# Performance work log

Measured on AMD Instinct MI355X. Metric: run time of the kernel, lower is better.

## Reference

```python
import jax, jax.numpy as jnp
import numpy as np

N_ETYPES = 6
N_STEPS = 5
N_ITERS = 6
N_LSTM_LAYERS = 3
NODES_PER_GRAPH = 200


def _uinit(key, shape, fan_in):
    s = 1.0 / np.sqrt(fan_in)
    return jax.random.uniform(key, shape, jnp.float32, -s, s)


def setup_inputs() -> dict:
    key = jax.random.key(0)
    ks = jax.random.split(key, 24)
    N, D = 64000, 64
    G = N // NODES_PER_GRAPH  # 320 graphs
    E = N * 16  # 1,024,000 edges
    feats = jax.random.normal(ks[0], (N, D), jnp.float32)
    # within-graph edges: local endpoint + graph offset
    graph_of_edge = jnp.repeat(jnp.arange(G, dtype=jnp.int32), E // G)
    src = jax.random.randint(ks[1], (E,), 0, NODES_PER_GRAPH, jnp.int32) + graph_of_edge * NODES_PER_GRAPH
    dst = jax.random.randint(ks[2], (E,), 0, NODES_PER_GRAPH, jnp.int32) + graph_of_edge * NODES_PER_GRAPH
    etypes = jax.random.randint(ks[3], (E,), 0, N_ETYPES, jnp.int32)
    node_graph = jnp.repeat(jnp.arange(G, dtype=jnp.int32), NODES_PER_GRAPH)
    # GatedGraphConv params: per-etype Linear(D,D) + GRUCell(D,D) (torch gate order r,z,n)
    W_edge = _uinit(ks[4], (N_ETYPES, D, D), D)
    b_edge = _uinit(ks[5], (N_ETYPES, D), D)
    gru_W_ih = _uinit(ks[6], (3 * D, D), D)
    gru_W_hh = _uinit(ks[7], (3 * D, D), D)
    gru_b_ih = _uinit(ks[8], (3 * D,), D)
    gru_b_hh = _uinit(ks[9], (3 * D,), D)
    # Set2Set LSTM: 3 layers, input 2D (layer0) / D (layers 1,2), hidden D; torch gate order i,f,g,o
    lstm_W_ih0 = _uinit(ks[10], (4 * D, 2 * D), D)
    lstm_W_hh0 = _uinit(ks[11], (4 * D, D), D)
    lstm_b_ih0 = _uinit(ks[12], (4 * D,), D)
    lstm_b_hh0 = _uinit(ks[13], (4 * D,), D)
    lstm_W_ih1 = _uinit(ks[14], (4 * D, D), D)
    lstm_W_hh1 = _uinit(ks[15], (4 * D, D), D)
    lstm_b_ih1 = _uinit(ks[16], (4 * D,), D)
    lstm_b_hh1 = _uinit(ks[17], (4 * D,), D)
    lstm_W_ih2 = _uinit(ks[18], (4 * D, D), D)
    lstm_W_hh2 = _uinit(ks[19], (4 * D, D), D)
    lstm_b_ih2 = _uinit(ks[20], (4 * D,), D)
    lstm_b_hh2 = _uinit(ks[21], (4 * D,), D)
    Wp = _uinit(ks[22], (3, 2 * D), 2 * D)
    bp = _uinit(ks[23], (3,), 2 * D)
    return dict(feats=feats, W_edge=W_edge, b_edge=b_edge,
                gru_W_ih=gru_W_ih, gru_W_hh=gru_W_hh, gru_b_ih=gru_b_ih, gru_b_hh=gru_b_hh,
                lstm_W_ih0=lstm_W_ih0, lstm_W_hh0=lstm_W_hh0, lstm_b_ih0=lstm_b_ih0, lstm_b_hh0=lstm_b_hh0,
                lstm_W_ih1=lstm_W_ih1, lstm_W_hh1=lstm_W_hh1, lstm_b_ih1=lstm_b_ih1, lstm_b_hh1=lstm_b_hh1,
                lstm_W_ih2=lstm_W_ih2, lstm_W_hh2=lstm_W_hh2, lstm_b_ih2=lstm_b_ih2, lstm_b_hh2=lstm_b_hh2,
                Wp=Wp, bp=bp, src=src, dst=dst, etypes=etypes, node_graph=node_graph)


def _ggnn_forward(feats, W_edge, b_edge, gru_W_ih, gru_W_hh, gru_b_ih, gru_b_hh,
                  lstm_params, Wp, bp, src, dst, etypes, node_graph):
    N, D = feats.shape
    G = N // NODES_PER_GRAPH
    h = feats
    # --- GatedGraphConv: 5 steps of etype-typed transform + scatter-sum + GRU ---
    for _ in range(N_STEPS):
        # transform every node by every etype weight (cheap: N << E), then gather per edge
        Wh = jnp.einsum('nd,tdo->tno', h, W_edge) + b_edge[:, None, :]  # [T,N,D]
        msg = Wh[etypes, src]                                           # [E,D] gather
        a = jax.ops.segment_sum(msg, dst, num_segments=N)               # [N,D] scatter-add
        gi = a @ gru_W_ih.T + gru_b_ih
        gh = h @ gru_W_hh.T + gru_b_hh
        i_r, i_z, i_n = jnp.split(gi, 3, -1)
        h_r, h_z, h_n = jnp.split(gh, 3, -1)
        r = jax.nn.sigmoid(i_r + h_r)
        z = jax.nn.sigmoid(i_z + h_z)
        n = jnp.tanh(i_n + r * h_n)
        h = (1.0 - z) * n + z * h
    feat = h
    # --- Set2Set readout ---
    q_star = jnp.zeros((G, 2 * D), feat.dtype)
    hs = jnp.zeros((N_LSTM_LAYERS, G, D), feat.dtype)
    cs = jnp.zeros((N_LSTM_LAYERS, G, D), feat.dtype)
    for _ in range(N_ITERS):
        x = q_star
        new_h, new_c = [], []
        for l, (Wi, Whh, bi, bh) in enumerate(lstm_params):
            gates = x @ Wi.T + bi + hs[l] @ Whh.T + bh
            ii, ff, gg, oo = jnp.split(gates, 4, -1)
            c = jax.nn.sigmoid(ff) * cs[l] + jax.nn.sigmoid(ii) * jnp.tanh(gg)
            x = jax.nn.sigmoid(oo) * jnp.tanh(c)
            new_h.append(x)
            new_c.append(c)
        hs = jnp.stack(new_h)
        cs = jnp.stack(new_c)
        q = x  # [G,D]
        e = jnp.sum(feat * q[node_graph], axis=-1)                         # [N]
        emax = jax.ops.segment_max(e, node_graph, num_segments=G)
        ex = jnp.exp(e - emax[node_graph])
        denom = jax.ops.segment_sum(ex, node_graph, num_segments=G)
        alpha = ex / denom[node_graph]                                     # segment softmax
        readout = jax.ops.segment_sum(feat * alpha[:, None], node_graph, num_segments=G)
        q_star = jnp.concatenate([q, readout], axis=-1)
    return q_star @ Wp.T + bp  # [G,3]


def reference(feats, W_edge, b_edge, gru_W_ih, gru_W_hh, gru_b_ih, gru_b_hh,
              lstm_W_ih0, lstm_W_hh0, lstm_b_ih0, lstm_b_hh0,
              lstm_W_ih1, lstm_W_hh1, lstm_b_ih1, lstm_b_hh1,
              lstm_W_ih2, lstm_W_hh2, lstm_b_ih2, lstm_b_hh2,
              Wp, bp, src, dst, etypes, node_graph):
    lstm_params = [
        (lstm_W_ih0, lstm_W_hh0, lstm_b_ih0, lstm_b_hh0),
        (lstm_W_ih1, lstm_W_hh1, lstm_b_ih1, lstm_b_hh1),
        (lstm_W_ih2, lstm_W_hh2, lstm_b_ih2, lstm_b_hh2),
    ]
    return _ggnn_forward(feats, W_edge, b_edge, gru_W_ih, gru_W_hh, gru_b_ih, gru_b_hh,
                         lstm_params, Wp, bp, src, dst, etypes, node_graph)
```

## Files before the change

### kernel.cpp

```cpp
#include <hip/hip_runtime.h>

typedef unsigned short u16;
typedef unsigned int u32;

#define DIM 64
#define NGRAPH 320
#define NPG 200
#define EPG 3200
#define EPG_P 5120
#define NSTEPS 5
#define NITERS 6
#define NTILES 13
#define NPAD 208
#define NTHR 1024

typedef __attribute__((ext_vector_type(8))) short bf16x8;
typedef __attribute__((ext_vector_type(4))) float f32x4;

__device__ __forceinline__ float bf2f(u16 u) {
  u32 x = ((u32)u) << 16;
  float f;
  __builtin_memcpy(&f, &x, 4);
  return f;
}
__device__ __forceinline__ u16 f2bf(float f) {
  u32 x;
  __builtin_memcpy(&x, &f, 4);
  x = (x + 0x7FFFu + ((x >> 16) & 1u)) >> 16;
  return (u16)x;
}
__device__ __forceinline__ float bflo(u32 w) {
  u32 x = w << 16;
  float f;
  __builtin_memcpy(&f, &x, 4);
  return f;
}
__device__ __forceinline__ float bfhi(u32 w) {
  u32 x = w & 0xffff0000u;
  float f;
  __builtin_memcpy(&f, &x, 4);
  return f;
}
__device__ __forceinline__ float sigmf(float x) { return 1.0f / (1.0f + __expf(-x)); }
__device__ __forceinline__ int swz(int row, int col) { return row * 64 + (col ^ ((row & 7) << 3)); }


__global__ void __launch_bounds__(256) k_csr(const int* __restrict__ src,
                                             const int* __restrict__ dst,
                                             const int* __restrict__ ety,
                                             u16* __restrict__ recs,
                                             int* __restrict__ rows) {
  __shared__ int cnt[3 * NPG];
  __shared__ int rofs[3 * (NPG + 1)];
  int g = blockIdx.x, tid = threadIdx.x;
  int base = g * NPG;
  for (int i = tid; i < 3 * NPG; i += 256) cnt[i] = 0;
  __syncthreads();
  for (int e = tid; e < EPG; e += 256) {
    int d = dst[g * EPG + e] - base;
    int t = ety[g * EPG + e];
    atomicAdd(&cnt[(t >> 1) * NPG + d], 1);
  }
  __syncthreads();
  if (tid == 0) {
    int s = 0;
    for (int p = 0; p < 3; p++) {
      for (int n = 0; n < NPG; n++) {
        rofs[p * (NPG + 1) + n] = s;
        s += (cnt[p * NPG + n] + 3) & ~3;
      }
      rofs[p * (NPG + 1) + NPG] = s;
    }
  }
  __syncthreads();
  for (int i = tid; i < 3 * NPG; i += 256) cnt[i] = rofs[(i / NPG) * (NPG + 1) + (i % NPG)];
  __syncthreads();
  for (int e = tid; e < EPG; e += 256) {
    int d = dst[g * EPG + e] - base;
    int t = ety[g * EPG + e];
    int sl = src[g * EPG + e] - base;
    int pos = atomicAdd(&cnt[(t >> 1) * NPG + d], 1);
    recs[(size_t)g * EPG_P + pos] = (u16)((t & 1) * NPAD + sl);
  }
  __syncthreads();
  for (int i = tid; i < 3 * NPG; i += 256) {
    int ph = i / NPG, n = i % NPG;
    int end = rofs[ph * (NPG + 1) + n + 1];
    for (int p = cnt[i]; p < end; p++) recs[(size_t)g * EPG_P + p] = (u16)NPG;
  }
  for (int i = tid; i < 3 * (NPG + 1); i += 256) rows[g * 3 * (NPG + 1) + i] = rofs[i];
}

__global__ void __launch_bounds__(256) k_prep(
    const float* __restrict__ W_edge, const float* __restrict__ gWih, const float* __restrict__ gWhh,
    const float* __restrict__ lWi0, const float* __restrict__ lWh0,
    const float* __restrict__ lWi1, const float* __restrict__ lWh1,
    const float* __restrict__ lWi2, const float* __restrict__ lWh2,
    u16* __restrict__ WeTb, u16* __restrict__ Wihb, u16* __restrict__ Whhb,
    u16* __restrict__ WTih0b, u16* __restrict__ WThh0b,
    u16* __restrict__ WTih1b, u16* __restrict__ WThh1b,
    u16* __restrict__ WTih2b, u16* __restrict__ WThh2b) {
  int i = blockIdx.x * 256 + threadIdx.x;
  if (i < 24576) {
    int t = i >> 12, rem = i & 4095, o = rem >> 6, k = rem & 63;
    WeTb[i] = f2bf(W_edge[t * 4096 + k * 64 + o]);
  } else if (i < 36864) {
    int idx = i - 24576;
    Wihb[idx] = f2bf(gWih[idx]);
  } else if (i < 49152) {
    int idx = i - 36864;
    Whhb[idx] = f2bf(gWhh[idx]);
  } else if (i < 81920) {
    int idx = i - 49152;
    int k = idx >> 8, jj = idx & 255;
    WTih0b[idx] = f2bf(lWi0[jj * 128 + k]);
  } else {
    int idx = i - 81920;
    int seg = idx >> 14;
    int r = idx & 16383;
    int k = r >> 8, jj = r & 255;
    const float* sp = seg == 0 ? lWh0 : seg == 1 ? lWi1 : seg == 2 ? lWh1 : seg == 3 ? lWi2 : lWh2;
    u16* dp = seg == 0 ? WThh0b : seg == 1 ? WTih1b : seg == 2 ? WThh1b : seg == 3 ? WTih2b : WThh2b;
    dp[r] = f2bf(sp[jj * 64 + k]);
  }
}


__global__ void __launch_bounds__(NTHR) k_ggnn(
    const float* __restrict__ feats,
    const u16* __restrict__ WeTb, const float* __restrict__ b_edge,
    const u16* __restrict__ Wihb, const u16* __restrict__ Whhb,
    const float* __restrict__ gbih, const float* __restrict__ gbhh,
    const u16* __restrict__ recs, const int* __restrict__ rows,
    const u16* __restrict__ WTih0b, const u16* __restrict__ WThh0b,
    const u16* __restrict__ WTih1b, const u16* __restrict__ WThh1b,
    const u16* __restrict__ WTih2b, const u16* __restrict__ WThh2b,
    const float* __restrict__ b_ih0, const float* __restrict__ b_hh0,
    const float* __restrict__ b_ih1, const float* __restrict__ b_hh1,
    const float* __restrict__ b_ih2, const float* __restrict__ b_hh2,
    const float* __restrict__ Wp, const float* __restrict__ bp,
    float* __restrict__ out) {
  __shared__ __align__(16) u16 hb_s[NPAD * 64];
  __shared__ __align__(16) u16 wh_s[2 * NPAD * 64];
  __shared__ __align__(16) float acc_s[NPG * 64];
  __shared__ __align__(16) char u_s[12656];

  u16* rec_s = (u16*)u_s;
  int* rows_s = (int*)(u_s + 10240);
  float* qstar = (float*)u_s;
  float* xbuf = (float*)(u_s + 512);
  float* hs_f = (float*)(u_s + 768);
  float* cs_f = (float*)(u_s + 1536);
  float* gates = (float*)(u_s + 2304);
  float* gpart = (float*)(u_s + 3328);
  float* e_s = (float*)(u_s + 7424);
  float* red_f = (float*)(u_s + 8224);
  float* scal = (float*)(u_s + 12320);

  int g = blockIdx.x, tid = threadIdx.x;
  int lane = tid & 63, wid = tid >> 6;
  int m = lane & 15, quad = lane >> 4;
  int half = lane >> 5, l32 = lane & 31;

  const float* fg = feats + (size_t)g * (NPG * 64);
  for (int i = tid; i < NPG * 64; i += NTHR) hb_s[swz(i >> 6, i & 63)] = f2bf(fg[i]);
  for (int i = tid; i < (NPAD - NPG) * 64; i += NTHR) hb_s[NPG * 64 + i] = 0;
  for (int i = tid; i < 2 * 8 * 64; i += NTHR) {
    int tl = i >> 9, rem = i & 511;
    wh_s[(tl * NPAD + NPG + (rem >> 6)) * 64 + (rem & 63)] = 0;
  }
  {
    const u32* r32 = (const u32*)(recs + (size_t)g * EPG_P);
    u32* rl = (u32*)rec_s;
    for (int i = tid; i < EPG_P / 2; i += NTHR) rl[i] = r32[i];
  }
  for (int i = tid; i < 3 * (NPG + 1); i += NTHR) rows_s[i] = rows[g * 3 * (NPG + 1) + i];

  float hreg[4][4] = {};
  if (wid < NTILES) {
#pragma unroll
    for (int r = 0; r < 4; r++) {
      int node = wid * 16 + quad * 4 + r;
      if (node < NPG) {
#pragma unroll
        for (int dq = 0; dq < 4; dq++) hreg[r][dq] = fg[node * 64 + dq * 16 + m];
      }
    }
  }

  u16* ab_s = wh_s;
  int ot = wid & 3, hh = wid >> 2;

#pragma unroll 1
  for (int step = 0; step < NSTEPS; step++) {
    __syncthreads();
    {
      float4* z4 = (float4*)acc_s;
      float4 z = {0.f, 0.f, 0.f, 0.f};
      for (int i = tid; i < NPG * 16; i += NTHR) z4[i] = z;
    }
#pragma unroll 1
    for (int ph = 0; ph < 3; ph++) {
      if (ph > 0) __syncthreads();
      {
        const u16* bp0 = WeTb + (((2 * ph) * 64 + ot * 16 + m) * 64) + quad * 8;
        const u16* bp1 = WeTb + (((2 * ph + 1) * 64 + ot * 16 + m) * 64) + quad * 8;
        bf16x8 B00 = *(const bf16x8*)bp0;
        bf16x8 B01 = *(const bf16x8*)(bp0 + 32);
        bf16x8 B10 = *(const bf16x8*)bp1;
        bf16x8 B11 = *(const bf16x8*)(bp1 + 32);
        float bias0 = b_edge[(2 * ph) * 64 + ot * 16 + m];
        float bias1 = b_edge[(2 * ph + 1) * 64 + ot * 16 + m];
        for (int nt = hh; nt < NTILES; nt += 4) {
          int arow = nt * 16 + m;
          bf16x8 a0 = *(const bf16x8*)(hb_s + swz(arow, quad * 8));
          bf16x8 a1 = *(const bf16x8*)(hb_s + swz(arow, quad * 8 + 32));
          f32x4 c = {0.f, 0.f, 0.f, 0.f};
          c = __builtin_amdgcn_mfma_f32_16x16x32_bf16(a0, B00, c, 0, 0, 0);
          c = __builtin_amdgcn_mfma_f32_16x16x32_bf16(a1, B01, c, 0, 0, 0);
#pragma unroll
          for (int r = 0; r < 4; r++) {
            int node = nt * 16 + quad * 4 + r;
            if (node < NPG) wh_s[node * 64 + ot * 16 + m] = f2bf(c[r] + bias0);
          }
        }
        for (int nt = 3 - hh; nt < NTILES; nt += 4) {
          int arow = nt * 16 + m;
          bf16x8 a0 = *(const bf16x8*)(hb_s + swz(arow, quad * 8));
          bf16x8 a1 = *(const bf16x8*)(hb_s + swz(arow, quad * 8 + 32));
          f32x4 c = {0.f, 0.f, 0.f, 0.f};
          c = __builtin_amdgcn_mfma_f32_16x16x32_bf16(a0, B10, c, 0, 0, 0);
          c = __builtin_amdgcn_mfma_f32_16x16x32_bf16(a1, B11, c, 0, 0, 0);
#pragma unroll
          for (int r = 0; r < 4; r++) {
            int node = nt * 16 + quad * 4 + r;
            if (node < NPG) wh_s[(NPAD + node) * 64 + ot * 16 + m] = f2bf(c[r] + bias1);
          }
        }
      }
      __syncthreads();
      const int* rowp = rows_s + ph * (NPG + 1);
      for (int q = 0; q < 13; q++) {
        int n = q * 16 + wid;
        if (n >= NPG) continue;
        int rs = rowp[n], re = rowp[n + 1];
        float r0 = 0.f, r1 = 0.f;
        for (int e = rs; e < re; e += 4) {
          int pA = rec_s[e + half];
          int pB = rec_s[e + 2 + half];
          u32 wA = *(const u32*)(wh_s + pA * 64 + 2 * l32);
          u32 wB = *(const u32*)(wh_s + pB * 64 + 2 * l32);
          r0 += bflo(wA) + bflo(wB);
          r1 += bfhi(wA) + bfhi(wB);
        }
        r0 += __shfl_xor(r0, 32);
        r1 += __shfl_xor(r1, 32);
        if (lane < 32) {
          float2* p = (float2*)(acc_s + n * 64 + 2 * l32);
          float2 v = *p;
          v.x += r0;
          v.y += r1;
          *p = v;
        }
      }
    }
    __syncthreads();
    for (int idx = tid; idx < NPG * 32; idx += NTHR) {
      int n = idx >> 5, jj = idx & 31;
      float2 v = *(const float2*)(acc_s + n * 64 + 2 * jj);
      u32 pk = (u32)f2bf(v.x) | ((u32)f2bf(v.y) << 16);
      *(u32*)(ab_s + n * 64 + ((2 * jj) ^ ((n & 7) << 3))) = pk;
    }
    __syncthreads();
    if (wid < NTILES) {
      int nt = wid;
      int arow = nt * 16 + m;
      bf16x8 aa0 = *(const bf16x8*)(ab_s + swz(arow, quad * 8));
      bf16x8 aa1 = *(const bf16x8*)(ab_s + swz(arow, quad * 8 + 32));
      bf16x8 ah0 = *(const bf16x8*)(hb_s + swz(arow, quad * 8));
      bf16x8 ah1 = *(const bf16x8*)(hb_s + swz(arow, quad * 8 + 32));
#pragma unroll
      for (int dq = 0; dq < 4; dq++) {
        int d = dq * 16 + m;
        f32x4 z4 = {0.f, 0.f, 0.f, 0.f};
        const u16* bi = Wihb + (dq * 16 + m) * 64 + quad * 8;
        const u16* bh = Whhb + (dq * 16 + m) * 64 + quad * 8;
        f32x4 cr = z4;
        {
          bf16x8 b0 = *(const bf16x8*)bi, b1 = *(const bf16x8*)(bi + 32);
          bf16x8 c0 = *(const bf16x8*)bh, c1 = *(const bf16x8*)(bh + 32);
          cr = __builtin_amdgcn_mfma_f32_16x16x32_bf16(ah0, c0, cr, 0, 0, 0);
          cr = __builtin_amdgcn_mfma_f32_16x16x32_bf16(ah1, c1, cr, 0, 0, 0);
          cr = __builtin_amdgcn_mfma_f32_16x16x32_bf16(aa0, b0, cr, 0, 0, 0);
          cr = __builtin_amdgcn_mfma_f32_16x16x32_bf16(aa1, b1, cr, 0, 0, 0);
        }
        const u16* bi2 = Wihb + ((4 + dq) * 16 + m) * 64 + quad * 8;
        const u16* bh2 = Whhb + ((4 + dq) * 16 + m) * 64 + quad * 8;
        f32x4 cz = z4;
        {
          bf16x8 b0 = *(const bf16x8*)bi2, b1 = *(const bf16x8*)(bi2 + 32);
          bf16x8 c0 = *(const bf16x8*)bh2, c1 = *(const bf16x8*)(bh2 + 32);
          cz = __builtin_amdgcn_mfma_f32_16x16x32_bf16(ah0, c0, cz, 0, 0, 0);
          cz = __builtin_amdgcn_mfma_f32_16x16x32_bf16(ah1, c1, cz, 0, 0, 0);
          cz = __builtin_amdgcn_mfma_f32_16x16x32_bf16(aa0, b0, cz, 0, 0, 0);
          cz = __builtin_amdgcn_mfma_f32_16x16x32_bf16(aa1, b1, cz, 0, 0, 0);
        }
        const u16* bi3 = Wihb + ((8 + dq) * 16 + m) * 64 + quad * 8;
        const u16* bh3 = Whhb + ((8 + dq) * 16 + m) * 64 + quad * 8;
        f32x4 ci = z4, ch = z4;
        {
          bf16x8 b0 = *(const bf16x8*)bi3, b1 = *(const bf16x8*)(bi3 + 32);
          bf16x8 c0 = *(const bf16x8*)bh3, c1 = *(const bf16x8*)(bh3 + 32);
          ci = __builtin_amdgcn_mfma_f32_16x16x32_bf16(aa0, b0, ci, 0, 0, 0);
          ci = __builtin_amdgcn_mfma_f32_16x16x32_bf16(aa1, b1, ci, 0, 0, 0);
          ch = __builtin_amdgcn_mfma_f32_16x16x32_bf16(ah0, c0, ch, 0, 0, 0);
          ch = __builtin_amdgcn_mfma_f32_16x16x32_bf16(ah1, c1, ch, 0, 0, 0);
        }
        float bi_r = gbih[d], bh_r = gbhh[d];
        float bi_z = gbih[64 + d], bh_z = gbhh[64 + d];
        float bi_n = gbih[128 + d], bh_n = gbhh[128 + d];
#pragma unroll
        for (int r = 0; r < 4; r++) {
          int node = nt * 16 + quad * 4 + r;
          if (node < NPG) {
            float rr = sigmf(cr[r] + bi_r + bh_r);
            float zz = sigmf(cz[r] + bi_z + bh_z);
            float nn = tanhf(ci[r] + bi_n + rr * (ch[r] + bh_n));
            float hv = hreg[r][dq];
            float hnew = (1.0f - zz) * nn + zz * hv;
            hreg[r][dq] = hnew;
            hb_s[swz(node, d)] = f2bf(hnew);
            if (step == NSTEPS - 1) acc_s[node * 64 + d] = hnew;
          }
        }
      }
    }
  }
  __syncthreads();
  const float* feat_s = acc_s;

  int j = tid & 255, part = tid >> 8;
  float bs0 = 0.f, bs1 = 0.f, bs2 = 0.f;
  if (tid < 256) {
    bs0 = b_ih0[tid] + b_hh0[tid];
    bs1 = b_ih1[tid] + b_hh1[tid];
    bs2 = b_ih2[tid] + b_hh2[tid];
  }
  __syncthreads();
  if (tid < 128) qstar[tid] = 0.f;
  if (tid < 64) {
    xbuf[tid] = 0.f;
    for (int l = 0; l < 3; l++) {
      hs_f[l * 64 + tid] = 0.f;
      cs_f[l * 64 + tid] = 0.f;
    }
  }
  __syncthreads();
#pragma unroll 1
  for (int it = 0; it < NITERS; it++) {
    {
      float a0 = 0.f;
      if (part == 0) {
#pragma unroll 8
        for (int k = 0; k < 48; k++) a0 += qstar[k] * bf2f(WTih0b[k * 256 + j]);
      } else if (part == 1) {
#pragma unroll 8
        for (int k = 48; k < 96; k++) a0 += qstar[k] * bf2f(WTih0b[k * 256 + j]);
      } else if (part == 2) {
#pragma unroll 8
        for (int k = 96; k < 128; k++) a0 += qstar[k] * bf2f(WTih0b[k * 256 + j]);
#pragma unroll 8
        for (int k = 0; k < 16; k++) a0 += hs_f[k] * bf2f(WThh0b[k * 256 + j]);
      } else {
#pragma unroll 8
        for (int k = 16; k < 64; k++) a0 += hs_f[k] * bf2f(WThh0b[k * 256 + j]);
      }
      gpart[part * 256 + j] = a0;
    }
    __syncthreads();
    if (tid < 256)
      gates[tid] = gpart[tid] + gpart[256 + tid] + gpart[512 + tid] + gpart[768 + tid] + bs0;
    __syncthreads();
    if (tid < 64) {
      float cc = sigmf(gates[64 + tid]) * cs_f[tid] + sigmf(gates[tid]) * tanhf(gates[128 + tid]);
      float x = sigmf(gates[192 + tid]) * tanhf(cc);
      cs_f[tid] = cc;
      hs_f[tid] = x;
      xbuf[tid] = x;
    }
    __syncthreads();
#pragma unroll 1
    for (int l = 1; l < 3; l++) {
      const u16* W = (l == 1) ? ((part < 2) ? WTih1b : WThh1b)
                              : ((part < 2) ? WTih2b : WThh2b);
      const float* xv = (part < 2) ? xbuf : (hs_f + l * 64);
      int k0 = (part & 1) * 32;
      float a0 = 0.f;
#pragma unroll 8
      for (int k = k0; k < k0 + 32; k++) a0 += xv[k] * bf2f(W[k * 256 + j]);
      gpart[part * 256 + j] = a0;
      __syncthreads();
      float bsl = (l == 1) ? bs1 : bs2;
      if (tid < 256)
        gates[tid] = gpart[tid] + gpart[256 + tid] + gpart[512 + tid] + gpart[768 + tid] + bsl;
      __syncthreads();
      if (tid < 64) {
        float cc = sigmf(gates[64 + tid]) * cs_f[l * 64 + tid] +
                   sigmf(gates[tid]) * tanhf(gates[128 + tid]);
        float x = sigmf(gates[192 + tid]) * tanhf(cc);
        cs_f[l * 64 + tid] = cc;
        hs_f[l * 64 + tid] = x;
        xbuf[tid] = x;
      }
      __syncthreads();
    }
    for (int n = wid; n < NPG; n += 16) {
      float v = feat_s[n * 64 + lane] * xbuf[lane];
      for (int off = 32; off > 0; off >>= 1) v += __shfl_down(v, off);
      if (lane == 0) e_s[n] = v;
    }
    __syncthreads();
    if (tid < 64) {
      float mx = -1e30f;
      for (int n = lane; n < NPG; n += 64) mx = fmaxf(mx, e_s[n]);
      for (int off = 32; off > 0; off >>= 1) mx = fmaxf(mx, __shfl_down(mx, off));
      mx = __shfl(mx, 0);
      float ssum = 0.f;
      for (int n = lane; n < NPG; n += 64) {
        float ex = __expf(e_s[n] - mx);
        e_s[n] = ex;
        ssum += ex;
      }
      for (int off = 32; off > 0; off >>= 1) ssum += __shfl_down(ssum, off);
      if (lane == 0) scal[0] = ssum;
    }
    __syncthreads();
    float denom = scal[0];
    {
      float r = 0.f;
      for (int n = wid; n < NPG; n += 16) r += feat_s[n * 64 + lane] * e_s[n];
      red_f[wid * 64 + lane] = r;
    }
    __syncthreads();
    if (tid < 64) {
      float ro = 0.f;
#pragma unroll
      for (int ww = 0; ww < 16; ww++) ro += red_f[ww * 64 + lane];
      qstar[lane] = xbuf[lane];
      qstar[64 + lane] = ro / denom;
    }
    __syncthreads();
  }
  if (tid < 3) {
    float s = bp[tid];
    for (int k = 0; k < 128; k++) s += qstar[k] * Wp[tid * 128 + k];
    out[g * 3 + tid] = s;
  }
}


extern "C" void kernel_launch(void* const* d_in, const int* in_sizes, int n_in,
                              void* d_out, int out_size, void* d_ws, size_t ws_size,
                              hipStream_t stream) {
  const float* feats  = (const float*)d_in[0];
  const float* W_edge = (const float*)d_in[1];
  const float* b_edge = (const float*)d_in[2];
  const float* gWih   = (const float*)d_in[3];
  const float* gWhh   = (const float*)d_in[4];
  const float* gbih   = (const float*)d_in[5];
  const float* gbhh   = (const float*)d_in[6];
  const float* lWi0   = (const float*)d_in[7];
  const float* lWh0   = (const float*)d_in[8];
  const float* lbi0   = (const float*)d_in[9];
  const float* lbh0   = (const float*)d_in[10];
  const float* lWi1   = (const float*)d_in[11];
  const float* lWh1   = (const float*)d_in[12];
  const float* lbi1   = (const float*)d_in[13];
  const float* lbh1   = (const float*)d_in[14];
  const float* lWi2   = (const float*)d_in[15];
  const float* lWh2   = (const float*)d_in[16];
  const float* lbi2   = (const float*)d_in[17];
  const float* lbh2   = (const float*)d_in[18];
  const float* Wp     = (const float*)d_in[19];
  const float* bp     = (const float*)d_in[20];
  const int* src      = (const int*)d_in[21];
  const int* dst      = (const int*)d_in[22];
  const int* ety      = (const int*)d_in[23];
  float* out = (float*)d_out;

  char* ws = (char*)d_ws;
  u16* recs    = (u16*)ws;
  int* rows    = (int*)(ws + 3276800);
  u16* WeTb    = (u16*)(ws + 4048640);
  u16* Wihb    = (u16*)(ws + 4097792);
  u16* Whhb    = (u16*)(ws + 4122368);
  u16* WTih0b  = (u16*)(ws + 4146944);
  u16* WThh0b  = (u16*)(ws + 4212480);
  u16* WTih1b  = (u16*)(ws + 4245248);
  u16* WThh1b  = (u16*)(ws + 4278016);
  u16* WTih2b  = (u16*)(ws + 4310784);
  u16* WThh2b  = (u16*)(ws + 4343552);

  k_csr<<<NGRAPH, 256, 0, stream>>>(src, dst, ety, recs, rows);
  k_prep<<<640, 256, 0, stream>>>(W_edge, gWih, gWhh, lWi0, lWh0, lWi1, lWh1, lWi2, lWh2,
                                  WeTb, Wihb, Whhb, WTih0b, WThh0b, WTih1b, WThh1b, WTih2b, WThh2b);
  k_ggnn<<<NGRAPH, NTHR, 0, stream>>>(feats, WeTb, b_edge, Wihb, Whhb, gbih, gbhh, recs, rows,
                                      WTih0b, WThh0b, WTih1b, WThh1b, WTih2b, WThh2b,
                                      lbi0, lbh0, lbi1, lbh1, lbi2, lbh2, Wp, bp, out);
}
```

Before: 803.9 us.

## Keep message accumulators in registers across etype phases; move GRU state to shared

Per-node gather sums now stay in 26 register accumulators per thread across the three etype phases, replacing read-modify-write into a float shared buffer. Each wave's results are written straight to the bf16 A-operand buffer in one flush. This drops the per-step zeroing pass and the separate float-to-bf16 conversion pass. To free registers, the fp32 hidden state moves from per-thread registers into a shared array that also serves as the final features, which costs extra shared-memory traffic in the GRU update.

```diff
diff --git a/kernel.cpp b/kernel.cpp
--- a/kernel.cpp
+++ b/kernel.cpp
@@ -43,6 +43,8 @@
 }
 __device__ __forceinline__ float sigmf(float x) { return 1.0f / (1.0f + __expf(-x)); }
 __device__ __forceinline__ int swz(int row, int col) { return row * 64 + (col ^ ((row & 7) << 3)); }
+
+#define REP13(M) M(0) M(1) M(2) M(3) M(4) M(5) M(6) M(7) M(8) M(9) M(10) M(11) M(12)
 
 
 __global__ void __launch_bounds__(256) k_csr(const int* __restrict__ src,
@@ -142,7 +144,7 @@
     float* __restrict__ out) {
   __shared__ __align__(16) u16 hb_s[NPAD * 64];
   __shared__ __align__(16) u16 wh_s[2 * NPAD * 64];
-  __shared__ __align__(16) float acc_s[NPG * 64];
+  __shared__ __align__(16) float h32_s[NPG * 64];
   __shared__ __align__(16) char u_s[12656];
 
   u16* rec_s = (u16*)u_s;
@@ -163,7 +165,11 @@
   int half = lane >> 5, l32 = lane & 31;
 
   const float* fg = feats + (size_t)g * (NPG * 64);
-  for (int i = tid; i < NPG * 64; i += NTHR) hb_s[swz(i >> 6, i & 63)] = f2bf(fg[i]);
+  for (int i = tid; i < NPG * 64; i += NTHR) {
+    float v = fg[i];
+    h32_s[i] = v;
+    hb_s[swz(i >> 6, i & 63)] = f2bf(v);
+  }
   for (int i = tid; i < (NPAD - NPG) * 64; i += NTHR) hb_s[NPG * 64 + i] = 0;
   for (int i = tid; i < 2 * 8 * 64; i += NTHR) {
     int tl = i >> 9, rem = i & 511;
@@ -176,32 +182,44 @@
   }
   for (int i = tid; i < 3 * (NPG + 1); i += NTHR) rows_s[i] = rows[g * 3 * (NPG + 1) + i];
 
-  float hreg[4][4] = {};
-  if (wid < NTILES) {
-#pragma unroll
-    for (int r = 0; r < 4; r++) {
-      int node = wid * 16 + quad * 4 + r;
-      if (node < NPG) {
-#pragma unroll
-        for (int dq = 0; dq < 4; dq++) hreg[r][dq] = fg[node * 64 + dq * 16 + m];
-      }
-    }
-  }
-
   u16* ab_s = wh_s;
   int ot = wid & 3, hh = wid >> 2;
 
+#define ACC_DECL(q) float a0_##q, a1_##q;
+  REP13(ACC_DECL)
+#define ACC_ZERO(q) a0_##q = 0.f; a1_##q = 0.f;
+#define GATHER(q)                                              \
+  {                                                            \
+    int n = (q)*16 + wid;                                      \
+    if (n < NPG) {                                             \
+      int rs = rowp[n], re = rowp[n + 1];                      \
+      for (int e = rs; e < re; e += 4) {                       \
+        int pA = rec_s[e + half];                              \
+        int pB = rec_s[e + 2 + half];                          \
+        u32 wA = *(const u32*)(wh_s + pA * 64 + 2 * l32);      \
+        u32 wB = *(const u32*)(wh_s + pB * 64 + 2 * l32);      \
+        a0_##q += bflo(wA) + bflo(wB);                         \
+        a1_##q += bfhi(wA) + bfhi(wB);                         \
+      }                                                        \
+    }                                                          \
+  }
+#define FLUSH(q)                                                   \
+  {                                                                \
+    int n = (q)*16 + wid;                                          \
+    float s0 = a0_##q + __shfl_xor(a0_##q, 32);                    \
+    float s1 = a1_##q + __shfl_xor(a1_##q, 32);                    \
+    if (n < NPG && lane < 32) {                                    \
+      u32 pk = (u32)f2bf(s0) | ((u32)f2bf(s1) << 16);              \
+      *(u32*)(ab_s + n * 64 + ((2 * l32) ^ ((n & 7) << 3))) = pk;  \
+    }                                                              \
+  }
+
 #pragma unroll 1
   for (int step = 0; step < NSTEPS; step++) {
-    __syncthreads();
-    {
-      float4* z4 = (float4*)acc_s;
-      float4 z = {0.f, 0.f, 0.f, 0.f};
-      for (int i = tid; i < NPG * 16; i += NTHR) z4[i] = z;
-    }
+    REP13(ACC_ZERO)
 #pragma unroll 1
     for (int ph = 0; ph < 3; ph++) {
-      if (ph > 0) __syncthreads();
+      __syncthreads();
       {
         const u16* bp0 = WeTb + (((2 * ph) * 64 + ot * 16 + m) * 64) + quad * 8;
         const u16* bp1 = WeTb + (((2 * ph + 1) * 64 + ot * 16 + m) * 64) + quad * 8;
@@ -240,37 +258,10 @@
       }
       __syncthreads();
       const int* rowp = rows_s + ph * (NPG + 1);
-      for (int q = 0; q < 13; q++) {
-        int n = q * 16 + wid;
-        if (n >= NPG) continue;
-        int rs = rowp[n], re = rowp[n + 1];
-        float r0 = 0.f, r1 = 0.f;
-        for (int e = rs; e < re; e += 4) {
-          int pA = rec_s[e + half];
-          int pB = rec_s[e + 2 + half];
-          u32 wA = *(const u32*)(wh_s + pA * 64 + 2 * l32);
-          u32 wB = *(const u32*)(wh_s + pB * 64 + 2 * l32);
-          r0 += bflo(wA) + bflo(wB);
-          r1 += bfhi(wA) + bfhi(wB);
-        }
-        r0 += __shfl_xor(r0, 32);
-        r1 += __shfl_xor(r1, 32);
-        if (lane < 32) {
-          float2* p = (float2*)(acc_s + n * 64 + 2 * l32);
-          float2 v = *p;
-          v.x += r0;
-          v.y += r1;
-          *p = v;
-        }
-      }
-    }
-    __syncthreads();
-    for (int idx = tid; idx < NPG * 32; idx += NTHR) {
-      int n = idx >> 5, jj = idx & 31;
-      float2 v = *(const float2*)(acc_s + n * 64 + 2 * jj);
-      u32 pk = (u32)f2bf(v.x) | ((u32)f2bf(v.y) << 16);
-      *(u32*)(ab_s + n * 64 + ((2 * jj) ^ ((n & 7) << 3))) = pk;
-    }
+      REP13(GATHER)
+    }
+    __syncthreads();
+    REP13(FLUSH)
     __syncthreads();
     if (wid < NTILES) {
       int nt = wid;
@@ -326,18 +317,17 @@
             float rr = sigmf(cr[r] + bi_r + bh_r);
             float zz = sigmf(cz[r] + bi_z + bh_z);
             float nn = tanhf(ci[r] + bi_n + rr * (ch[r] + bh_n));
-            float hv = hreg[r][dq];
+            float hv = h32_s[node * 64 + d];
             float hnew = (1.0f - zz) * nn + zz * hv;
-            hreg[r][dq] = hnew;
+            h32_s[node * 64 + d] = hnew;
             hb_s[swz(node, d)] = f2bf(hnew);
-            if (step == NSTEPS - 1) acc_s[node * 64 + d] = hnew;
           }
         }
       }
     }
   }
   __syncthreads();
-  const float* feat_s = acc_s;
+  const float* feat_s = h32_s;
 
   int j = tid & 255, part = tid >> 8;
   float bs0 = 0.f, bs1 = 0.f, bs2 = 0.f;
```

Measured after the change: 706.0 us. 12.2% less time.
